# Optimization experiments

Measured on AMD Instinct MI355X. Metric: run time of the kernel, lower is better.

The kernel has to match this reference:

```python
import jax, jax.numpy as jnp
import numpy as np

N_NODES = 50000
N_EDGES = 800000
HEADS = 5
NFEAT = 5
C1 = 32  # hidden_layers


def setup_inputs() -> dict:
    key = jax.random.key(0)
    ks = jax.random.split(key, 20)
    s = 0.3  # glorot-ish scale
    d = {
        "x": jax.random.normal(ks[0], (N_NODES, NFEAT), jnp.float32),
        "edge_attr": jax.random.uniform(ks[1], (N_EDGES, 1), jnp.float32),
        "src": jax.random.randint(ks[2], (N_EDGES,), 0, N_NODES, jnp.int32),
        "dst": jax.random.randint(ks[3], (N_EDGES,), 0, N_NODES, jnp.int32),
        # conv1: in=5 -> heads=5, out=32, concat
        "W1": jax.random.normal(ks[4], (NFEAT, HEADS * C1), jnp.float32) * s,
        "a_src1": jax.random.normal(ks[5], (HEADS, C1), jnp.float32) * s,
        "a_dst1": jax.random.normal(ks[6], (HEADS, C1), jnp.float32) * s,
        "We1": jax.random.normal(ks[7], (1, HEADS * C1), jnp.float32) * s,
        "ae1": jax.random.normal(ks[8], (HEADS, C1), jnp.float32) * s,
        "b1": jnp.zeros((HEADS * C1,), jnp.float32),
        # conv2: in=160 -> heads=5, out=1, mean over heads
        "W2": jax.random.normal(ks[9], (HEADS * C1, HEADS * 1), jnp.float32) * 0.08,
        "a_src2": jax.random.normal(ks[10], (HEADS, 1), jnp.float32) * s,
        "a_dst2": jax.random.normal(ks[11], (HEADS, 1), jnp.float32) * s,
        "We2": jax.random.normal(ks[12], (1, HEADS * 1), jnp.float32) * s,
        "ae2": jax.random.normal(ks[13], (HEADS, 1), jnp.float32) * s,
        "b2": jnp.zeros((1,), jnp.float32),
        "Wlin": jax.random.normal(ks[14], (1, 1), jnp.float32),
    }
    return d


def gat_layer(x, src, dst, eattr, W, a_src, a_dst, We, a_e, bias, concat, n_nodes):
    """PyG GATConv with edge_dim, self-loops already added by caller."""
    H, C = a_src.shape
    h = (x @ W).reshape(-1, H, C)                      # [N,H,C]
    alpha_s = (h * a_src[None]).sum(-1)                # [N,H]
    alpha_d = (h * a_dst[None]).sum(-1)                # [N,H]
    ee = (eattr @ We).reshape(-1, H, C)                # [E,H,C]
    alpha_e = (ee * a_e[None]).sum(-1)                 # [E,H]
    logits = jax.nn.leaky_relu(alpha_s[src] + alpha_d[dst] + alpha_e, 0.2)
    # segment softmax over destination nodes
    m = jax.ops.segment_max(logits, dst, num_segments=n_nodes)
    m = jnp.where(jnp.isfinite(m), m, 0.0)
    ex = jnp.exp(logits - m[dst])
    denom = jax.ops.segment_sum(ex, dst, num_segments=n_nodes)
    alpha = ex / (denom[dst] + 1e-16)                  # [E,H]
    msg = (alpha[:, :, None] * h[src]).reshape(-1, H * C)
    agg = jax.ops.segment_sum(msg, dst, num_segments=n_nodes).reshape(n_nodes, H, C)
    if concat:
        return agg.reshape(n_nodes, H * C) + bias
    return agg.mean(axis=1) + bias


def reference(x, edge_attr, src, dst, W1, a_src1, a_dst1, We1, ae1, b1,
              W2, a_src2, a_dst2, We2, ae2, b2, Wlin):
    n = x.shape[0]
    loop = jnp.arange(n, dtype=src.dtype)
    s = jnp.concatenate([src, loop])
    t = jnp.concatenate([dst, loop])
    # self-loop edge_attr = mean of edge_attr (PyG fill_value='mean')
    ea_loop = jnp.broadcast_to(edge_attr.mean(axis=0, keepdims=True), (n, edge_attr.shape[1]))
    ea = jnp.concatenate([edge_attr, ea_loop], axis=0)

    x1 = gat_layer(x, s, t, ea, W1, a_src1, a_dst1, We1, ae1, b1, True, n)
    x2 = jax.nn.relu(x1)
    # dropout p=0.2 is identity in eval mode
    x4 = gat_layer(x2, s, t, ea, W2, a_src2, a_dst2, We2, ae2, b2, False, n)
    x5 = x4 @ Wlin                                     # Linear(1,1,bias=False)
    return jax.nn.sigmoid(x5)                          # [N,1]
```

## Files before the change

### kernel.cpp

```cpp
#include <hip/hip_runtime.h>
#include <hip/hip_fp16.h>
#include <math.h>

#define N_NODES 50000
#define N_EDGES 800000
#define E2 (N_EDGES + N_NODES)
#define HEADS 5
#define C1 32
#define F1 160

#define BSZ 64
#define NBK 782
#define NBL 128
#define CH  6641
#define MTOT (NBK*NBL)
#define MC  391
#define GRID_H1 1563
#define CAP 1408

#define AGG1_NPB 32
#define AGG1_NB  1563

static constexpr size_t alignup(size_t x){ return (x + 255) & ~size_t(255); }
static constexpr size_t OFF_SCAL  = 0;
static constexpr size_t OFF_H     = alignup(OFF_SCAL + 64*4);
static constexpr size_t OFF_EAS   = alignup(OFF_H    + (size_t)MTOT*4);
static constexpr size_t OFF_PART  = alignup(OFF_EAS  + (size_t)NBL*4);
static constexpr size_t OFF_PPREF = alignup(OFF_PART + (size_t)MC*4);
static constexpr size_t OFF_BST   = alignup(OFF_PPREF+ (size_t)MC*4);
static constexpr size_t OFF_OFFS  = alignup(OFF_BST  + (size_t)(NBK+1)*4);
static constexpr size_t OFF_BPACK = alignup(OFF_OFFS + (size_t)(N_NODES+1)*4);
static constexpr size_t OFF_EDG   = alignup(OFF_BPACK+ (size_t)E2*8);
static constexpr size_t OFF_AS16  = alignup(OFF_EDG  + (size_t)E2*4);
static constexpr size_t OFF_AD16  = alignup(OFF_AS16 + (size_t)N_NODES*8*2);
static constexpr size_t OFF_G16   = alignup(OFF_AD16 + (size_t)N_NODES*8*2);
static constexpr size_t OFF_AD2P  = alignup(OFF_G16  + (size_t)N_NODES*16*2);
static constexpr size_t OFF_H1Q   = alignup(OFF_AD2P + (size_t)N_NODES*8*4);
static constexpr size_t OFF_P01   = alignup(OFF_H1Q  + (size_t)N_NODES*F1);
static constexpr size_t OFF_P2    = alignup(OFF_P01  + (size_t)2*E2*4);
static constexpr size_t OFF_H2A   = alignup(OFF_P2   + (size_t)3*E2*4);

typedef float vf2 __attribute__((ext_vector_type(2)));
__device__ __forceinline__ float4 fp8x4_to_f32(unsigned int r){
  vf2 lo = __builtin_amdgcn_cvt_pk_f32_fp8((int)r, false);
  vf2 hi = __builtin_amdgcn_cvt_pk_f32_fp8((int)r, true);
  return make_float4(lo.x, lo.y, hi.x, hi.y);
}

__global__ __launch_bounds__(320) void k_init(const float* __restrict__ x, const float* __restrict__ W1,
                       const float* __restrict__ as1w, const float* __restrict__ ad1w,
                       unsigned short* __restrict__ h1qh, __half* __restrict__ as16, __half* __restrict__ ad16,
                       const int* __restrict__ dst, const float* __restrict__ ea,
                       int* __restrict__ H, float* __restrict__ easum){
  __shared__ float sW[5*F1];
  __shared__ float sx[32*5];
  int t = threadIdx.x;
  if (blockIdx.x < GRID_H1){
    for (int k = t; k < 5*F1; k += 320) sW[k] = W1[k];
    int xb = blockIdx.x*160;
    if (t < 160 && xb + t < N_NODES*5) sx[t] = x[xb + t];
    __syncthreads();
    int nl = t / 80;
    int c  = t - nl*80;
    int c0 = 2*c;
    int hh = c >> 4, pp = c & 15;
    float w0[5], w1[5];
    #pragma unroll
    for (int f = 0; f < 5; f++){ w0[f] = sW[f*F1 + c0]; w1[f] = sW[f*F1 + c0 + 1]; }
    float aw0 = as1w[c0], aw1 = as1w[c0+1];
    float dw0 = ad1w[c0], dw1 = ad1w[c0+1];
    #pragma unroll
    for (int it = 0; it < 8; it++){
      int n = blockIdx.x*32 + it*4 + nl;
      if (n < N_NODES){
        const float* xv = sx + (it*4 + nl)*5;
        float hv0 = 0.f, hv1 = 0.f;
        #pragma unroll
        for (int f = 0; f < 5; f++){
          hv0 += xv[f] * w0[f];
          hv1 += xv[f] * w1[f];
        }
        int pk = __builtin_amdgcn_cvt_pk_fp8_f32(hv0, hv1, 0, false);
        h1qh[(size_t)hh*(N_NODES*16) + n*16 + pp] = (unsigned short)(pk & 0xFFFF);
        float vs = hv0*aw0 + hv1*aw1;
        float vd = hv0*dw0 + hv1*dw1;
        #pragma unroll
        for (int m = 8; m >= 1; m >>= 1){
          vs += __shfl_xor(vs, m, 64);
          vd += __shfl_xor(vd, m, 64);
        }
        if ((c & 15) == 0){
          int h = c >> 4;
          as16[n*8 + h] = __float2half(vs);
          ad16[n*8 + h] = __float2half(vd);
        }
      }
    }
  } else {
    int* hist = (int*)sW;
    float* wsum = (float*)&hist[NBK + 1];
    for (int k = t; k < NBK; k += 320) hist[k] = 0;
    __syncthreads();
    int b = blockIdx.x - GRID_H1;
    int e0 = b*CH, e1 = min(e0 + CH, E2);
    float s = 0.f;
    for (int e = e0 + t; e < e1; e += 320){
      int d;
      if (e < N_EDGES){ d = dst[e]; s += ea[e]; }
      else d = e - N_EDGES;
      atomicAdd(&hist[d >> 6], 1);
    }
    #pragma unroll
    for (int m = 1; m < 64; m <<= 1) s += __shfl_xor(s, m, 64);
    if ((t & 63) == 0) wsum[t >> 6] = s;
    __syncthreads();
    for (int k = t; k < NBK; k += 320) H[(size_t)k*NBL + b] = hist[k];
    if (t == 0) easum[b] = wsum[0] + wsum[1] + wsum[2] + wsum[3] + wsum[4];
  }
}

__global__ void k_s1(const int* __restrict__ H, int* __restrict__ partial,
                     float* __restrict__ h2acc){
  int i = blockIdx.x*256 + threadIdx.x;
  for (int z = i; z < N_NODES*HEADS; z += MC*256) h2acc[z] = 0.f;
  int v = (i < MTOT) ? H[i] : 0;
  #pragma unroll
  for (int m = 1; m < 64; m <<= 1) v += __shfl_xor(v, m, 64);
  __shared__ int sh[4];
  if ((threadIdx.x & 63) == 0) sh[threadIdx.x >> 6] = v;
  __syncthreads();
  if (threadIdx.x == 0) partial[blockIdx.x] = sh[0] + sh[1] + sh[2] + sh[3];
}

__global__ __launch_bounds__(512) void k_s2p(const int* __restrict__ partial, int* __restrict__ ppref,
                      int* __restrict__ offs, int* __restrict__ bstart,
                      const float* __restrict__ easum,
                      const float* __restrict__ We1, const float* __restrict__ ae1,
                      const float* __restrict__ We2, const float* __restrict__ ae2,
                      float* __restrict__ scal){
  __shared__ int sp[512];
  __shared__ float sh_ea[NBL];
  int t = threadIdx.x;
  if (t < NBL) sh_ea[t] = easum[t];
  if (t >= 448 && t < 448 + HEADS){
    int h = t - 448;
    float s = 0.f;
    for (int c = 0; c < C1; c++) s += We1[h*C1 + c] * ae1[h*C1 + c];
    scal[2 + h] = s;
    scal[7 + h] = We2[h] * ae2[h];
  }
  int v = (t < MC) ? partial[t] : 0;
  sp[t] = v;
  __syncthreads();
  if (t == 511){
    float es = 0.f;
    for (int i = 0; i < NBL; i++) es += sh_ea[i];
    scal[1] = es / (float)N_EDGES;
  }
  for (int off = 1; off < 512; off <<= 1){
    int u = (t >= off) ? sp[t - off] : 0;
    __syncthreads();
    sp[t] += u;
    __syncthreads();
  }
  if (t < MC) ppref[t] = sp[t] - v;
  if (t == 0){ offs[N_NODES] = E2; bstart[NBK] = E2; }
}

__global__ void k_s3(int* __restrict__ H, const int* __restrict__ ppref, int* __restrict__ bstart){
  __shared__ int sp[256];
  int b = blockIdx.x, t = threadIdx.x;
  int i = b*256 + t;
  int v = (i < MTOT) ? H[i] : 0;
  sp[t] = v;
  __syncthreads();
  for (int off = 1; off < 256; off <<= 1){
    int u = (t >= off) ? sp[t - off] : 0;
    __syncthreads();
    sp[t] += u;
    __syncthreads();
  }
  int P = ppref[b] + sp[t] - v;
  if (i < MTOT){
    H[i] = P;
    if (i % NBL == 0) bstart[i / NBL] = P;
  }
}

__global__ __launch_bounds__(256) void k_scat(const int* __restrict__ src, const int* __restrict__ dst,
                       const float* __restrict__ ea, const float* __restrict__ scal,
                       const int* __restrict__ H, int2* __restrict__ bpack){
  __shared__ int lofs[NBK];
  int b = blockIdx.x;
  for (int k = threadIdx.x; k < NBK; k += 256) lofs[k] = H[(size_t)k*NBL + b];
  __syncthreads();
  float mean = scal[1];
  int e0 = b*CH, e1 = min(e0 + CH, E2);
  for (int e = e0 + threadIdx.x; e < e1; e += 256){
    int d, s; float a;
    if (e < N_EDGES){ d = dst[e]; s = src[e]; a = ea[e]; }
    else { d = s = e - N_EDGES; a = mean; }
    int pos = atomicAdd(&lofs[d >> 6], 1);
    bpack[pos] = make_int2(s | ((d & 63) << 16), __float_as_int(a));
  }
}

__global__ __launch_bounds__(256) void k_final2(const int* __restrict__ bstart,
                        const int2* __restrict__ bpack,
                        const __half* __restrict__ as16, const __half* __restrict__ ad16,
                        const float* __restrict__ scal,
                        int* __restrict__ offs, unsigned int* __restrict__ edge2,
                        unsigned int* __restrict__ P01, unsigned int* __restrict__ P2){
  __shared__ int cnt[BSZ], cur[BSZ];
  __shared__ unsigned int s_edge[CAP];
  __shared__ unsigned char s_d6[CAP];
  __shared__ float sAd[HEADS][BSZ];
  int k = blockIdx.x, t = threadIdx.x;
  int base = k*BSZ;
  if (t < BSZ){
    cnt[t] = 0;
    int n = base + t;
    uint4 adu = make_uint4(0,0,0,0);
    if (n < N_NODES) adu = *(const uint4*)(ad16 + (size_t)n*8);
    union { uint4 u; __half2 h[4]; } AD; AD.u = adu;
    sAd[0][t] = __low2float(AD.h[0]); sAd[1][t] = __high2float(AD.h[0]);
    sAd[2][t] = __low2float(AD.h[1]); sAd[3][t] = __high2float(AD.h[1]);
    sAd[4][t] = __low2float(AD.h[2]);
  }
  __syncthreads();
  int r0 = bstart[k], r1 = bstart[k + 1];
  int sz = r1 - r0;
  for (int j = r0 + t; j < r1; j += 256) atomicAdd(&cnt[(bpack[j].x >> 16) & 63], 1);
  __syncthreads();
  if (t == 0){
    int run = 0;
    for (int i = 0; i < BSZ; i++){ int c = cnt[i]; cnt[i] = run; cur[i] = run; run += c; }
  }
  __syncthreads();
  if (t < BSZ){
    int n = base + t;
    if (n < N_NODES) offs[n] = r0 + cnt[t];
  }
  float wd0 = scal[2], wd1 = scal[3], wd2 = scal[4], wd3 = scal[5], wd4 = scal[6];
  if (sz <= CAP){
    for (int j = r0 + t; j < r1; j += 256){
      int2 v = bpack[j];
      int d6 = (v.x >> 16) & 63;
      int lp = atomicAdd(&cur[d6], 1);
      s_edge[lp] = (unsigned int)(v.x & 0xFFFF) |
                   ((unsigned int)__half_as_ushort(__float2half(__int_as_float(v.y))) << 16);
      s_d6[lp] = (unsigned char)d6;
    }
    __syncthreads();
    for (int i = t; i < sz; i += 256){
      unsigned int e = s_edge[i];
      unsigned int lo = e & 0xFFFFu;
      int s = (int)lo;
      int d6 = s_d6[i];
      float c = __half2float(__ushort_as_half((unsigned short)(e >> 16)));
      union { uint4 u; __half2 h[4]; } AS; AS.u = *(const uint4*)(as16 + (size_t)s*8);
      float l0 = __low2float(AS.h[0])  + sAd[0][d6] + c*wd0;  l0 = fminf(fmaxf(l0, 0.2f*l0), 10.f);
      float l1 = __high2float(AS.h[0]) + sAd[1][d6] + c*wd1;  l1 = fminf(fmaxf(l1, 0.2f*l1), 10.f);
      float l2 = __low2float(AS.h[1])  + sAd[2][d6] + c*wd2;  l2 = fminf(fmaxf(l2, 0.2f*l2), 10.f);
      float l3 = __high2float(AS.h[1]) + sAd[3][d6] + c*wd3;  l3 = fminf(fmaxf(l3, 0.2f*l3), 10.f);
      float l4 = __low2float(AS.h[2])  + sAd[4][d6] + c*wd4;  l4 = fminf(fmaxf(l4, 0.2f*l4), 10.f);
      unsigned int p0 = (unsigned int)__half_as_ushort(__float2half(__expf(l0)));
      unsigned int p1 = (unsigned int)__half_as_ushort(__float2half(__expf(l1)));
      unsigned int p2 = (unsigned int)__half_as_ushort(__float2half(__expf(l2)));
      unsigned int p3 = (unsigned int)__half_as_ushort(__float2half(__expf(l3)));
      unsigned int p4 = (unsigned int)__half_as_ushort(__float2half(__expf(l4)));
      int pos = r0 + i;
      edge2[pos]               = e;
      P01[pos]                 = lo | (p0 << 16);
      P01[(size_t)E2 + pos]    = lo | (p1 << 16);
      P2[pos]                  = lo | (p2 << 16);
      P2[(size_t)E2 + pos]     = lo | (p3 << 16);
      P2[(size_t)2*E2 + pos]   = lo | (p4 << 16);
    }
  } else {
    for (int j = r0 + t; j < r1; j += 256){
      int2 v = bpack[j];
      int d6 = (v.x >> 16) & 63;
      int pos = r0 + atomicAdd(&cur[d6], 1);
      int s = v.x & 0xFFFF;
      float c = __int_as_float(v.y);
      unsigned int lo = (unsigned int)s;
      unsigned int e = lo | ((unsigned int)__half_as_ushort(__float2half(c)) << 16);
      union { uint4 u; __half2 h[4]; } AS; AS.u = *(const uint4*)(as16 + (size_t)s*8);
      float l0 = __low2float(AS.h[0])  + sAd[0][d6] + c*wd0;  l0 = fminf(fmaxf(l0, 0.2f*l0), 10.f);
      float l1 = __high2float(AS.h[0]) + sAd[1][d6] + c*wd1;  l1 = fminf(fmaxf(l1, 0.2f*l1), 10.f);
      float l2 = __low2float(AS.h[1])  + sAd[2][d6] + c*wd2;  l2 = fminf(fmaxf(l2, 0.2f*l2), 10.f);
      float l3 = __high2float(AS.h[1]) + sAd[3][d6] + c*wd3;  l3 = fminf(fmaxf(l3, 0.2f*l3), 10.f);
      float l4 = __low2float(AS.h[2])  + sAd[4][d6] + c*wd4;  l4 = fminf(fmaxf(l4, 0.2f*l4), 10.f);
      edge2[pos]               = e;
      P01[pos]                 = lo | ((unsigned int)__half_as_ushort(__float2half(__expf(l0))) << 16);
      P01[(size_t)E2 + pos]    = lo | ((unsigned int)__half_as_ushort(__float2half(__expf(l1))) << 16);
      P2[pos]                  = lo | ((unsigned int)__half_as_ushort(__float2half(__expf(l2))) << 16);
      P2[(size_t)E2 + pos]     = lo | ((unsigned int)__half_as_ushort(__float2half(__expf(l3))) << 16);
      P2[(size_t)2*E2 + pos]   = lo | ((unsigned int)__half_as_ushort(__float2half(__expf(l4))) << 16);
    }
  }
}

__global__ __launch_bounds__(256) void k_agg1(const int* __restrict__ offs,
                      const unsigned int* __restrict__ P01, const unsigned int* __restrict__ P2,
                      const unsigned short* __restrict__ h1qh,
                      const float* __restrict__ b1, const float* __restrict__ W2,
                      float* __restrict__ h2acc){
  int head = blockIdx.x / AGG1_NB;
  int nb   = blockIdx.x - head*AGG1_NB;
  __shared__ float sW2[C1*HEADS];
  for (int i = threadIdx.x; i < C1*HEADS; i += 256) sW2[i] = W2[head*C1*HEADS + i];
  __syncthreads();
  int gl   = threadIdx.x >> 3;
  int q    = threadIdx.x & 7;
  int n    = nb*AGG1_NPB + gl;
  if (n >= N_NODES) return;
  const unsigned int* EP = (head < 2) ? (P01 + (size_t)head*E2)
                                      : (P2  + (size_t)(head-2)*E2);
  const unsigned int* h1row = (const unsigned int*)h1qh + (size_t)head*(N_NODES*8) + q;
  int j0 = offs[n], j1 = offs[n + 1];
  float a0 = 0.f, a1 = 0.f, a2 = 0.f, a3 = 0.f, den = 0.f;
  int j = j0;
  for (; j + 7 < j1; j += 8){
    uint4 sa = *(const uint4*)(EP + j);
    uint4 sb = *(const uint4*)(EP + j + 4);
    unsigned int e0 = sa.x, e1 = sa.y, e2v = sa.z, e3 = sa.w;
    unsigned int e4 = sb.x, e5 = sb.y, e6 = sb.z, e7 = sb.w;
    int s0 = e0 & 0xFFFF, s1 = e1 & 0xFFFF, s2 = e2v & 0xFFFF, s3 = e3 & 0xFFFF;
    int s4 = e4 & 0xFFFF, s5 = e5 & 0xFFFF, s6 = e6 & 0xFFFF, s7 = e7 & 0xFFFF;
    unsigned int r0 = h1row[s0*8];
    unsigned int r1 = h1row[s1*8];
    unsigned int r2 = h1row[s2*8];
    unsigned int r3 = h1row[s3*8];
    unsigned int r4 = h1row[s4*8];
    unsigned int r5 = h1row[s5*8];
    unsigned int r6 = h1row[s6*8];
    unsigned int r7 = h1row[s7*8];
    float p0 = __half2float(__ushort_as_half((unsigned short)(e0 >> 16)));
    float p1 = __half2float(__ushort_as_half((unsigned short)(e1 >> 16)));
    float p2 = __half2float(__ushort_as_half((unsigned short)(e2v >> 16)));
    float p3 = __half2float(__ushort_as_half((unsigned short)(e3 >> 16)));
    float p4 = __half2float(__ushort_as_half((unsigned short)(e4 >> 16)));
    float p5 = __half2float(__ushort_as_half((unsigned short)(e5 >> 16)));
    float p6 = __half2float(__ushort_as_half((unsigned short)(e6 >> 16)));
    float p7 = __half2float(__ushort_as_half((unsigned short)(e7 >> 16)));
    den += ((p0 + p1) + (p2 + p3)) + ((p4 + p5) + (p6 + p7));
    float4 f0 = fp8x4_to_f32(r0), f1 = fp8x4_to_f32(r1);
    float4 f2 = fp8x4_to_f32(r2), f3 = fp8x4_to_f32(r3);
    float4 f4 = fp8x4_to_f32(r4), f5 = fp8x4_to_f32(r5);
    float4 f6 = fp8x4_to_f32(r6), f7 = fp8x4_to_f32(r7);
    a0 += p0*f0.x; a1 += p0*f0.y; a2 += p0*f0.z; a3 += p0*f0.w;
    a0 += p1*f1.x; a1 += p1*f1.y; a2 += p1*f1.z; a3 += p1*f1.w;
    a0 += p2*f2.x; a1 += p2*f2.y; a2 += p2*f2.z; a3 += p2*f2.w;
    a0 += p3*f3.x; a1 += p3*f3.y; a2 += p3*f3.z; a3 += p3*f3.w;
    a0 += p4*f4.x; a1 += p4*f4.y; a2 += p4*f4.z; a3 += p4*f4.w;
    a0 += p5*f5.x; a1 += p5*f5.y; a2 += p5*f5.z; a3 += p5*f5.w;
    a0 += p6*f6.x; a1 += p6*f6.y; a2 += p6*f6.z; a3 += p6*f6.w;
    a0 += p7*f7.x; a1 += p7*f7.y; a2 += p7*f7.z; a3 += p7*f7.w;
  }
  for (; j < j1; ++j){
    unsigned int e = EP[j];
    int s = e & 0xFFFF;
    float p = __half2float(__ushort_as_half((unsigned short)(e >> 16)));
    den += p;
    float4 f = fp8x4_to_f32(h1row[s*8]);
    a0 += p*f.x; a1 += p*f.y; a2 += p*f.z; a3 += p*f.w;
  }
  float inv = 1.f / (den + 1e-16f);
  float4 bb = *(const float4*)(b1 + head*C1 + 4*q);
  float v0 = fmaxf(a0*inv + bb.x, 0.f);
  float v1 = fmaxf(a1*inv + bb.y, 0.f);
  float v2 = fmaxf(a2*inv + bb.z, 0.f);
  float v3 = fmaxf(a3*inv + bb.w, 0.f);
  const float* wr = sW2 + (4*q)*HEADS;
  float hh[HEADS];
  #pragma unroll
  for (int h2i = 0; h2i < HEADS; h2i++)
    hh[h2i] = v0*wr[0*HEADS + h2i] + v1*wr[1*HEADS + h2i]
            + v2*wr[2*HEADS + h2i] + v3*wr[3*HEADS + h2i];
  #pragma unroll
  for (int m = 1; m < 8; m <<= 1){
    #pragma unroll
    for (int h2i = 0; h2i < HEADS; h2i++) hh[h2i] += __shfl_xor(hh[h2i], m, 8);
  }
  if (q == 0){
    #pragma unroll
    for (int h2i = 0; h2i < HEADS; h2i++)
      atomicAdd(&h2acc[n*HEADS + h2i], hh[h2i]);
  }
}

__global__ __launch_bounds__(256) void k_h2b(const float* __restrict__ h2acc,
                    const float* __restrict__ asw2, const float* __restrict__ adw2,
                    __half* __restrict__ G16, float* __restrict__ ad2p){
  int n = blockIdx.x*256 + threadIdx.x;
  if (n >= N_NODES) return;
  float a0 = h2acc[n*HEADS + 0], a1 = h2acc[n*HEADS + 1], a2 = h2acc[n*HEADS + 2];
  float a3 = h2acc[n*HEADS + 3], a4 = h2acc[n*HEADS + 4];
  float s0 = asw2[0], s1 = asw2[1], s2 = asw2[2], s3 = asw2[3], s4 = asw2[4];
  __half2 g0 = __floats2half2_rn(a0, a1);
  __half2 g1 = __floats2half2_rn(a2, a3);
  __half2 g2 = __floats2half2_rn(a4, a0*s0);
  __half2 g3 = __floats2half2_rn(a1*s1, a2*s2);
  __half2 g4 = __floats2half2_rn(a3*s3, a4*s4);
  __half2 z  = __floats2half2_rn(0.f, 0.f);
  uint4 lo = make_uint4(*(unsigned int*)&g0, *(unsigned int*)&g1,
                        *(unsigned int*)&g2, *(unsigned int*)&g3);
  uint4 hi = make_uint4(*(unsigned int*)&g4, *(unsigned int*)&z,
                        *(unsigned int*)&z,  *(unsigned int*)&z);
  *(uint4*)(G16 + (size_t)n*16)     = lo;
  *(uint4*)(G16 + (size_t)n*16 + 8) = hi;
  float4 d0 = make_float4(a0*adw2[0], a1*adw2[1], a2*adw2[2], a3*adw2[3]);
  float4 d1 = make_float4(a4*adw2[4], 0.f, 0.f, 0.f);
  *(float4*)(ad2p + (size_t)n*8)     = d0;
  *(float4*)(ad2p + (size_t)n*8 + 4) = d1;
}

__global__ __launch_bounds__(256) void k_agg2(const int* __restrict__ offs,
                      const unsigned int* __restrict__ edge2,
                      const __half* __restrict__ G16, const float* __restrict__ ad2p,
                      const float* __restrict__ scal,
                      const float* __restrict__ b2, const float* __restrict__ Wlin,
                      float* __restrict__ out){
  int grp = threadIdx.x >> 4;
  int l16 = threadIdx.x & 15;
  int n = blockIdx.x*16 + grp;
  float adn[HEADS], wd[HEADS];
  #pragma unroll
  for (int h = 0; h < HEADS; h++){ adn[h] = ad2p[n*8 + h]; wd[h] = scal[7 + h]; }
  int j0 = offs[n], j1 = offs[n + 1];

  float den[HEADS] = {0,0,0,0,0};
  float ac[HEADS]  = {0,0,0,0,0};
  for (int j = j0 + l16; j < j1; j += 16){
    unsigned int e = edge2[j];
    int s = e & 0xFFFF;
    float c = __half2float(__ushort_as_half((unsigned short)(e >> 16)));
    const __half* gs = G16 + (size_t)s*16;
    union { uint4 u; __half2 h[4]; } U; U.u = *(const uint4*)gs;
    union { uint2 u; __half2 h[2]; } V; V.u = *(const uint2*)(gs + 8);
    float2 p01 = __half22float2(U.h[0]);
    float2 p23 = __half22float2(U.h[1]);
    float2 p45 = __half22float2(U.h[2]);
    float2 p67 = __half22float2(U.h[3]);
    float2 p89 = __half22float2(V.h[0]);
    float hv[HEADS] = {p01.x, p01.y, p23.x, p23.y, p45.x};
    float av[HEADS] = {p45.y, p67.x, p67.y, p89.x, p89.y};
    #pragma unroll
    for (int h = 0; h < HEADS; h++){
      float lg = av[h] + adn[h] + c*wd[h];
      lg = fmaxf(lg, 0.2f*lg);
      lg = fminf(lg, 50.f);
      float p = __expf(lg);
      den[h] += p;
      ac[h]  += p * hv[h];
    }
  }
  #pragma unroll
  for (int m = 1; m < 16; m <<= 1){
    #pragma unroll
    for (int h = 0; h < HEADS; h++){
      den[h] += __shfl_xor(den[h], m, 16);
      ac[h]  += __shfl_xor(ac[h], m, 16);
    }
  }
  if (l16 == 0){
    float v = 0.f;
    #pragma unroll
    for (int h = 0; h < HEADS; h++) v += ac[h] / (den[h] + 1e-16f);
    v = v * (1.f/HEADS) + b2[0];
    v *= Wlin[0];
    out[n] = 1.f / (1.f + __expf(-v));
  }
}

extern "C" void kernel_launch(void* const* d_in, const int* in_sizes, int n_in,
                              void* d_out, int out_size, void* d_ws, size_t ws_size,
                              hipStream_t stream) {
  const float* x    = (const float*)d_in[0];
  const float* ea   = (const float*)d_in[1];
  const int*   src  = (const int*)d_in[2];
  const int*   dst  = (const int*)d_in[3];
  const float* W1   = (const float*)d_in[4];
  const float* as1w = (const float*)d_in[5];
  const float* ad1w = (const float*)d_in[6];
  const float* We1  = (const float*)d_in[7];
  const float* ae1  = (const float*)d_in[8];
  const float* b1   = (const float*)d_in[9];
  const float* W2   = (const float*)d_in[10];
  const float* as2w = (const float*)d_in[11];
  const float* ad2w = (const float*)d_in[12];
  const float* We2  = (const float*)d_in[13];
  const float* ae2  = (const float*)d_in[14];
  const float* b2   = (const float*)d_in[15];
  const float* Wlin = (const float*)d_in[16];

  char* ws = (char*)d_ws;
  float* scal   = (float*)(ws + OFF_SCAL);
  int*   H      = (int*)  (ws + OFF_H);
  float* easum  = (float*)(ws + OFF_EAS);
  int*   part   = (int*)  (ws + OFF_PART);
  int*   ppref  = (int*)  (ws + OFF_PPREF);
  int*   bstart = (int*)  (ws + OFF_BST);
  int*   offs   = (int*)  (ws + OFF_OFFS);
  int2*  bpack  = (int2*) (ws + OFF_BPACK);
  unsigned int* edge2 = (unsigned int*)(ws + OFF_EDG);
  unsigned int* P01 = (unsigned int*)(ws + OFF_P01);
  unsigned int* P2  = (unsigned int*)(ws + OFF_P2);
  __half* as16  = (__half*)(ws + OFF_AS16);
  __half* ad16  = (__half*)(ws + OFF_AD16);
  __half* G16   = (__half*)(ws + OFF_G16);
  float* ad2p   = (float*)(ws + OFF_AD2P);
  unsigned short* h1qh = (unsigned short*)(ws + OFF_H1Q);
  float* h2acc  = (float*)(ws + OFF_H2A);
  float* outp   = (float*)d_out;

  k_init   <<<GRID_H1 + NBL, 320, 0, stream>>>(x, W1, as1w, ad1w, h1qh, as16, ad16,
                                               dst, ea, H, easum);
  k_s1     <<<MC, 256, 0, stream>>>(H, part, h2acc);
  k_s2p    <<<1, 512, 0, stream>>>(part, ppref, offs, bstart, easum, We1, ae1, We2, ae2, scal);
  k_s3     <<<MC, 256, 0, stream>>>(H, ppref, bstart);
  k_scat   <<<NBL, 256, 0, stream>>>(src, dst, ea, scal, H, bpack);
  k_final2 <<<NBK, 256, 0, stream>>>(bstart, bpack, as16, ad16, scal, offs, edge2, P01, P2);

  k_agg1   <<<HEADS*AGG1_NB, 256, 0, stream>>>(offs, P01, P2, h1qh, b1, W2, h2acc);
  k_h2b    <<<(N_NODES + 255)/256, 256, 0, stream>>>(h2acc, as2w, ad2w, G16, ad2p);
  k_agg2   <<<N_NODES/16, 256, 0, stream>>>(offs, edge2, G16, ad2p, scal, b2, Wlin, outp);
}
```

Baseline: 199.8 us.

## Sort nodes by in-degree to balance work in aggregation kernels

Builds a degree histogram in k_final2, prefix-sums it, and scatters node ids into a degree-sorted permutation. The two aggregation kernels then process nodes in that order, so the lanes of a warp get segments of similar length and waste less time on divergence. The cost is two extra small kernel launches plus the atomics. Nodes are also no longer visited in index order, which scatters the accesses to per-node rows and outputs.

```diff
diff --git a/kernel.cpp b/kernel.cpp
--- a/kernel.cpp
+++ b/kernel.cpp
@@ -39,6 +39,8 @@
 static constexpr size_t OFF_P01   = alignup(OFF_H1Q  + (size_t)N_NODES*F1);
 static constexpr size_t OFF_P2    = alignup(OFF_P01  + (size_t)2*E2*4);
 static constexpr size_t OFF_H2A   = alignup(OFF_P2   + (size_t)3*E2*4);
+static constexpr size_t OFF_DBIN  = alignup(OFF_H2A  + (size_t)N_NODES*HEADS*4);
+static constexpr size_t OFF_PERM  = alignup(OFF_DBIN + 256*4);
 
 typedef float vf2 __attribute__((ext_vector_type(2)));
 __device__ __forceinline__ float4 fp8x4_to_f32(unsigned int r){
@@ -120,9 +122,10 @@
 }
 
 __global__ void k_s1(const int* __restrict__ H, int* __restrict__ partial,
-                     float* __restrict__ h2acc){
+                     float* __restrict__ h2acc, int* __restrict__ dbin){
   int i = blockIdx.x*256 + threadIdx.x;
   for (int z = i; z < N_NODES*HEADS; z += MC*256) h2acc[z] = 0.f;
+  if (i < 256) dbin[i] = 0;
   int v = (i < MTOT) ? H[i] : 0;
   #pragma unroll
   for (int m = 1; m < 64; m <<= 1) v += __shfl_xor(v, m, 64);
@@ -210,7 +213,8 @@
                         const __half* __restrict__ as16, const __half* __restrict__ ad16,
                         const float* __restrict__ scal,
                         int* __restrict__ offs, unsigned int* __restrict__ edge2,
-                        unsigned int* __restrict__ P01, unsigned int* __restrict__ P2){
+                        unsigned int* __restrict__ P01, unsigned int* __restrict__ P2,
+                        int* __restrict__ dbin){
   __shared__ int cnt[BSZ], cur[BSZ];
   __shared__ unsigned int s_edge[CAP];
   __shared__ unsigned char s_d6[CAP];
@@ -300,13 +304,51 @@
       P2[(size_t)2*E2 + pos]   = lo | ((unsigned int)__half_as_ushort(__float2half(__expf(l4))) << 16);
     }
   }
+  __syncthreads();
+  int* dh = (int*)s_edge;
+  if (t < 128) dh[t] = 0;
+  __syncthreads();
+  if (t < BSZ){
+    int n = base + t;
+    if (n < N_NODES){
+      int dend = (t < BSZ-1) ? cnt[t+1] : sz;
+      int deg = dend - cnt[t];
+      atomicAdd(&dh[min(deg, 127)], 1);
+    }
+  }
+  __syncthreads();
+  if (t < 128 && dh[t]) atomicAdd(&dbin[t], dh[t]);
+}
+
+__global__ __launch_bounds__(128) void k_ds(const int* __restrict__ dbin, int* __restrict__ dcur){
+  __shared__ int sp[128];
+  int t = threadIdx.x;
+  int v = dbin[t];
+  sp[t] = v;
+  __syncthreads();
+  for (int off = 1; off < 128; off <<= 1){
+    int u = (t >= off) ? sp[t - off] : 0;
+    __syncthreads();
+    sp[t] += u;
+    __syncthreads();
+  }
+  dcur[t] = sp[t] - v;
+}
+
+__global__ __launch_bounds__(256) void k_dp(const int* __restrict__ offs,
+                      int* __restrict__ dcur, int* __restrict__ perm){
+  int n = blockIdx.x*256 + threadIdx.x;
+  if (n >= N_NODES) return;
+  int deg = offs[n+1] - offs[n];
+  int pos = atomicAdd(&dcur[min(deg, 127)], 1);
+  perm[pos] = n;
 }
 
 __global__ __launch_bounds__(256) void k_agg1(const int* __restrict__ offs,
                       const unsigned int* __restrict__ P01, const unsigned int* __restrict__ P2,
                       const unsigned short* __restrict__ h1qh,
                       const float* __restrict__ b1, const float* __restrict__ W2,
-                      float* __restrict__ h2acc){
+                      const int* __restrict__ perm, float* __restrict__ h2acc){
   int head = blockIdx.x / AGG1_NB;
   int nb   = blockIdx.x - head*AGG1_NB;
   __shared__ float sW2[C1*HEADS];
@@ -314,8 +356,9 @@
   __syncthreads();
   int gl   = threadIdx.x >> 3;
   int q    = threadIdx.x & 7;
-  int n    = nb*AGG1_NPB + gl;
-  if (n >= N_NODES) return;
+  int idx  = nb*AGG1_NPB + gl;
+  if (idx >= N_NODES) return;
+  int n = perm[idx];
   const unsigned int* EP = (head < 2) ? (P01 + (size_t)head*E2)
                                       : (P2  + (size_t)(head-2)*E2);
   const unsigned int* h1row = (const unsigned int*)h1qh + (size_t)head*(N_NODES*8) + q;
@@ -420,12 +463,12 @@
 __global__ __launch_bounds__(256) void k_agg2(const int* __restrict__ offs,
                       const unsigned int* __restrict__ edge2,
                       const __half* __restrict__ G16, const float* __restrict__ ad2p,
-                      const float* __restrict__ scal,
+                      const float* __restrict__ scal, const int* __restrict__ perm,
                       const float* __restrict__ b2, const float* __restrict__ Wlin,
                       float* __restrict__ out){
   int grp = threadIdx.x >> 4;
   int l16 = threadIdx.x & 15;
-  int n = blockIdx.x*16 + grp;
+  int n = perm[blockIdx.x*16 + grp];
   float adn[HEADS], wd[HEADS];
   #pragma unroll
   for (int h = 0; h < HEADS; h++){ adn[h] = ad2p[n*8 + h]; wd[h] = scal[7 + h]; }
@@ -514,17 +557,22 @@
   float* ad2p   = (float*)(ws + OFF_AD2P);
   unsigned short* h1qh = (unsigned short*)(ws + OFF_H1Q);
   float* h2acc  = (float*)(ws + OFF_H2A);
+  int*   dbin   = (int*)  (ws + OFF_DBIN);
+  int*   dcur   = dbin + 128;
+  int*   perm   = (int*)  (ws + OFF_PERM);
   float* outp   = (float*)d_out;
 
   k_init   <<<GRID_H1 + NBL, 320, 0, stream>>>(x, W1, as1w, ad1w, h1qh, as16, ad16,
                                                dst, ea, H, easum);
-  k_s1     <<<MC, 256, 0, stream>>>(H, part, h2acc);
+  k_s1     <<<MC, 256, 0, stream>>>(H, part, h2acc, dbin);
   k_s2p    <<<1, 512, 0, stream>>>(part, ppref, offs, bstart, easum, We1, ae1, We2, ae2, scal);
   k_s3     <<<MC, 256, 0, stream>>>(H, ppref, bstart);
   k_scat   <<<NBL, 256, 0, stream>>>(src, dst, ea, scal, H, bpack);
-  k_final2 <<<NBK, 256, 0, stream>>>(bstart, bpack, as16, ad16, scal, offs, edge2, P01, P2);
-
-  k_agg1   <<<HEADS*AGG1_NB, 256, 0, stream>>>(offs, P01, P2, h1qh, b1, W2, h2acc);
+  k_final2 <<<NBK, 256, 0, stream>>>(bstart, bpack, as16, ad16, scal, offs, edge2, P01, P2, dbin);
+  k_ds     <<<1, 128, 0, stream>>>(dbin, dcur);
+  k_dp     <<<(N_NODES + 255)/256, 256, 0, stream>>>(offs, dcur, perm);
+
+  k_agg1   <<<HEADS*AGG1_NB, 256, 0, stream>>>(offs, P01, P2, h1qh, b1, W2, perm, h2acc);
   k_h2b    <<<(N_NODES + 255)/256, 256, 0, stream>>>(h2acc, as2w, ad2w, G16, ad2p);
-  k_agg2   <<<N_NODES/16, 256, 0, stream>>>(offs, edge2, G16, ad2p, scal, b2, Wlin, outp);
-}
+  k_agg2   <<<N_NODES/16, 256, 0, stream>>>(offs, edge2, G16, ad2p, scal, perm, b2, Wlin, outp);
+}
```

New measurement: 372.2 us. 86.3% more time.
